# Kernel tuning notes

Hardware: AMD Instinct MI355X
Metric: run time of the kernel (lower is better)

## Reference

```python
import jax, jax.numpy as jnp
import numpy as np

NUM_HEADS = 12

def setup_inputs() -> dict:
    key = jax.random.key(0)
    k1, k2, k3 = jax.random.split(key, 3)
    B, N, C = 8, 1024, 768
    x = jax.random.normal(k1, (B, N, C), dtype=jnp.float32)
    w_qkv = jax.random.normal(k2, (C, 3 * C), dtype=jnp.float32) * (C ** -0.5)
    w_proj = jax.random.normal(k3, (C, C), dtype=jnp.float32) * (C ** -0.5)
    b_proj = jnp.zeros((C,), dtype=jnp.float32)
    return {"x": x, "w_qkv": w_qkv, "w_proj": w_proj, "b_proj": b_proj}

def reference(x, w_qkv, w_proj, b_proj):
    B, N, C = x.shape
    H = NUM_HEADS
    D = C // H  # head_dim
    qkv = jnp.einsum('bnc,ce->bne', x, w_qkv)  # [B,N,3C]
    qkv = qkv.reshape(B, N, 3, H, D).transpose(2, 0, 3, 1, 4)  # [3,B,H,N,D]
    q, k, v = qkv[0], qkv[1], qkv[2]
    scale = D ** -0.5
    att = jax.nn.softmax(jnp.einsum('bhnd,bhmd->bhnm', q, k) * scale, axis=-1)
    out = jnp.einsum('bhnm,bhmd->bhnd', att, v)  # [B,H,N,D]
    out = out.transpose(0, 2, 1, 3).reshape(B, N, C)
    return jnp.einsum('bnc,cd->bnd', out, w_proj) + b_proj
```

## Files before the change

kernel.cpp:

```cpp
#include <hip/hip_runtime.h>

constexpr int Bb = 8, Nn = 1024, Cc = 768, Hh = 12, Dd = 64;
constexpr int Mtot = Bb * Nn;
constexpr int QKVN = 3 * Cc;
constexpr int BH = Bb * Hh;

typedef __attribute__((ext_vector_type(8))) short short8b;
typedef __attribute__((ext_vector_type(4))) float f32x4;
typedef __attribute__((ext_vector_type(4))) unsigned short u16x4;

__device__ inline unsigned short bf16_hi(float f) {
  unsigned int u = __float_as_uint(f);
  unsigned int r = (u + 0x7FFFu + ((u >> 16) & 1u)) >> 16;
  return (unsigned short)r;
}
__device__ inline float bf16_to_f32(unsigned short h) {
  return __uint_as_float(((unsigned int)h) << 16);
}

__global__ __launch_bounds__(256)
void transpose_split(const float* __restrict__ in, unsigned short* __restrict__ Th,
                     unsigned short* __restrict__ Tl, int K, int N) {
  __shared__ float tile[32][33];
  const int tx = threadIdx.x & 31;
  const int ty = threadIdx.x >> 5;
  const int gk = blockIdx.y * 32;
  const int gn = blockIdx.x * 32;

  #pragma unroll
  for (int i = 0; i < 4; ++i) {
    int k = gk + ty + 8 * i;
    tile[ty + 8 * i][tx] = in[(size_t)k * N + gn + tx];
  }
  __syncthreads();
  #pragma unroll
  for (int i = 0; i < 4; ++i) {
    int n = gn + ty + 8 * i;
    float v = tile[tx][ty + 8 * i];
    unsigned short h = bf16_hi(v);
    float fl = v - bf16_to_f32(h);
    Th[(size_t)n * K + gk + tx] = h;
    Tl[(size_t)n * K + gk + tx] = bf16_hi(fl);
  }
}

template <int EPI>
__global__ __launch_bounds__(256)
void gemm_mfma(const float* __restrict__ A, const unsigned short* __restrict__ BTh,
               const unsigned short* __restrict__ BTl, const float* __restrict__ bias,
               float* __restrict__ Cout, int K, int Ncols) {
  constexpr int LDH = 40;
  __shared__ unsigned short Ah[128][LDH], Al[128][LDH];
  __shared__ unsigned short Bh[128][LDH], Bl[128][LDH];

  const int tid = threadIdx.x;
  const int lane = tid & 63;
  const int w = tid >> 6;
  const int wm = (w & 1) * 64, wn = (w >> 1) * 64;
  const int m0 = blockIdx.y * 128, n0 = blockIdx.x * 128;

  const int srow = tid >> 1;
  const int sko = (tid & 1) * 16;

  f32x4 acc[4][4];
  #pragma unroll
  for (int i = 0; i < 4; ++i)
    #pragma unroll
    for (int j = 0; j < 4; ++j) acc[i][j] = (f32x4)0.f;

  const int lr = lane & 15;
  const int lk = (lane >> 4) * 8;

  for (int k0 = 0; k0 < K; k0 += 32) {
    __syncthreads();
    {
      const float* ap = &A[(size_t)(m0 + srow) * K + k0 + sko];
      #pragma unroll
      for (int i = 0; i < 4; ++i) {
        float4 v = *(const float4*)&ap[4 * i];
        u16x4 h, l;
        float f[4] = {v.x, v.y, v.z, v.w};
        #pragma unroll
        for (int e = 0; e < 4; ++e) {
          unsigned short hh = bf16_hi(f[e]);
          h[e] = hh;
          l[e] = bf16_hi(f[e] - bf16_to_f32(hh));
        }
        *(u16x4*)&Ah[srow][sko + 4 * i] = h;
        *(u16x4*)&Al[srow][sko + 4 * i] = l;
      }
    }
    {
      const unsigned short* bhp = &BTh[(size_t)(n0 + srow) * K + k0 + sko];
      const unsigned short* blp = &BTl[(size_t)(n0 + srow) * K + k0 + sko];
      *(short8b*)&Bh[srow][sko]     = *(const short8b*)bhp;
      *(short8b*)&Bh[srow][sko + 8] = *(const short8b*)(bhp + 8);
      *(short8b*)&Bl[srow][sko]     = *(const short8b*)blp;
      *(short8b*)&Bl[srow][sko + 8] = *(const short8b*)(blp + 8);
    }
    __syncthreads();

    short8b ahf[4], alf[4], bhf[4], blf[4];
    #pragma unroll
    for (int mi = 0; mi < 4; ++mi) {
      ahf[mi] = *(const short8b*)&Ah[wm + mi * 16 + lr][lk];
      alf[mi] = *(const short8b*)&Al[wm + mi * 16 + lr][lk];
    }
    #pragma unroll
    for (int nj = 0; nj < 4; ++nj) {
      bhf[nj] = *(const short8b*)&Bh[wn + nj * 16 + lr][lk];
      blf[nj] = *(const short8b*)&Bl[wn + nj * 16 + lr][lk];
    }
    #pragma unroll
    for (int mi = 0; mi < 4; ++mi)
      #pragma unroll
      for (int nj = 0; nj < 4; ++nj) {
        acc[mi][nj] = __builtin_amdgcn_mfma_f32_16x16x32_bf16(
            ahf[mi], bhf[nj], acc[mi][nj], 0, 0, 0);
        acc[mi][nj] = __builtin_amdgcn_mfma_f32_16x16x32_bf16(
            ahf[mi], blf[nj], acc[mi][nj], 0, 0, 0);
        acc[mi][nj] = __builtin_amdgcn_mfma_f32_16x16x32_bf16(
            alf[mi], bhf[nj], acc[mi][nj], 0, 0, 0);
      }
  }

  #pragma unroll
  for (int mi = 0; mi < 4; ++mi) {
    #pragma unroll
    for (int nj = 0; nj < 4; ++nj) {
      #pragma unroll
      for (int r = 0; r < 4; ++r) {
        int m = m0 + wm + mi * 16 + (lane >> 4) * 4 + r;
        int n = n0 + wn + nj * 16 + lr;
        float v = acc[mi][nj][r];
        if (EPI == 0) {
          int t = n0 / Cc;
          int rem = n - t * Cc;
          int h = rem >> 6, d = rem & 63;
          int bI = m >> 10, nI = m & 1023;
          Cout[(((size_t)t * BH + bI * Hh + h) * Nn + nI) * Dd + d] = v;
        } else {
          Cout[(size_t)m * Cc + n] = v + bias[n];
        }
      }
    }
  }
}

__global__ __launch_bounds__(256)
void attn_mfma(const float* __restrict__ qkv_ws, float* __restrict__ aout) {
  constexpr int LDH2 = 72;
  __shared__ unsigned short Qh[64][LDH2], Ql[64][LDH2];
  __shared__ unsigned short Ksh[64][LDH2], Ksl[64][LDH2];
  __shared__ unsigned short Vth[64][LDH2], Vtl[64][LDH2];
  __shared__ unsigned short Ph[64][LDH2], Pl[64][LDH2];

  const int bid = blockIdx.x;
  const int bh = bid >> 4, qt = bid & 15;
  const int b = bh / Hh, h = bh % Hh;
  const int tid = threadIdx.x;
  const int lane = tid & 63;
  const int wv = tid >> 6;
  const int q0 = wv * 16;
  const int qp = lane & 15;
  const int g  = lane >> 4;

  const float* Qg = qkv_ws + ((size_t)bh * Nn + qt * 64) * Dd;
  const float* Kg = qkv_ws + ((size_t)(BH + bh) * Nn) * Dd;
  const float* Vg = qkv_ws + ((size_t)(2 * BH + bh) * Nn) * Dd;
  const float scale = 0.125f;

  #pragma unroll
  for (int s = 0; s < 4; ++s) {
    int f = s * 256 + tid;
    int row = f >> 4, c4 = (f & 15) * 4;
    float4 v = *(const float4*)&Qg[row * 64 + c4];
    float fv[4] = {v.x, v.y, v.z, v.w};
    u16x4 hh, ll;
    #pragma unroll
    for (int e = 0; e < 4; ++e) {
      unsigned short x = bf16_hi(fv[e]);
      hh[e] = x; ll[e] = bf16_hi(fv[e] - bf16_to_f32(x));
    }
    *(u16x4*)&Qh[row][c4] = hh;
    *(u16x4*)&Ql[row][c4] = ll;
  }
  __syncthreads();
  short8b qfh[2], qfl[2];
  #pragma unroll
  for (int ks = 0; ks < 2; ++ks) {
    qfh[ks] = *(const short8b*)&Qh[q0 + qp][ks * 32 + g * 8];
    qfl[ks] = *(const short8b*)&Ql[q0 + qp][ks * 32 + g * 8];
  }

  f32x4 acc_o[4];
  #pragma unroll
  for (int dt = 0; dt < 4; ++dt) acc_o[dt] = (f32x4)0.f;
  float mrun = -1e30f, lrun = 0.f;

  for (int kt = 0; kt < 16; ++kt) {
    __syncthreads();
    #pragma unroll
    for (int s = 0; s < 4; ++s) {
      int f = s * 256 + tid;
      int row = f >> 4, c4 = (f & 15) * 4;
      float4 v = *(const float4*)&Kg[(size_t)(kt * 64 + row) * 64 + c4];
      float fv[4] = {v.x, v.y, v.z, v.w};
      u16x4 hh, ll;
      #pragma unroll
      for (int e = 0; e < 4; ++e) {
        unsigned short x = bf16_hi(fv[e]);
        hh[e] = x; ll[e] = bf16_hi(fv[e] - bf16_to_f32(x));
      }
      *(u16x4*)&Ksh[row][c4] = hh;
      *(u16x4*)&Ksl[row][c4] = ll;
    }
    #pragma unroll
    for (int s = 0; s < 2; ++s) {
      int f = s * 256 + tid;
      int kv2 = (f >> 4) * 2, c4 = (f & 15) * 4;
      float4 v0 = *(const float4*)&Vg[(size_t)(kt * 64 + kv2) * 64 + c4];
      float4 v1 = *(const float4*)&Vg[(size_t)(kt * 64 + kv2 + 1) * 64 + c4];
      float a0[4] = {v0.x, v0.y, v0.z, v0.w};
      float a1[4] = {v1.x, v1.y, v1.z, v1.w};
      #pragma unroll
      for (int e = 0; e < 4; ++e) {
        unsigned short h0 = bf16_hi(a0[e]), h1 = bf16_hi(a1[e]);
        unsigned short l0 = bf16_hi(a0[e] - bf16_to_f32(h0));
        unsigned short l1 = bf16_hi(a1[e] - bf16_to_f32(h1));
        *(unsigned int*)&Vth[c4 + e][kv2] = (unsigned)h0 | ((unsigned)h1 << 16);
        *(unsigned int*)&Vtl[c4 + e][kv2] = (unsigned)l0 | ((unsigned)l1 << 16);
      }
    }
    __syncthreads();

    f32x4 sacc[4];
    #pragma unroll
    for (int kb = 0; kb < 4; ++kb) sacc[kb] = (f32x4)0.f;
    #pragma unroll
    for (int kb = 0; kb < 4; ++kb) {
      #pragma unroll
      for (int ks = 0; ks < 2; ++ks) {
        short8b kfh = *(const short8b*)&Ksh[kb * 16 + qp][ks * 32 + g * 8];
        short8b kfl = *(const short8b*)&Ksl[kb * 16 + qp][ks * 32 + g * 8];
        sacc[kb] = __builtin_amdgcn_mfma_f32_16x16x32_bf16(kfh, qfh[ks], sacc[kb], 0, 0, 0);
        sacc[kb] = __builtin_amdgcn_mfma_f32_16x16x32_bf16(kfh, qfl[ks], sacc[kb], 0, 0, 0);
        sacc[kb] = __builtin_amdgcn_mfma_f32_16x16x32_bf16(kfl, qfh[ks], sacc[kb], 0, 0, 0);
      }
    }

    float sv[16];
    #pragma unroll
    for (int kb = 0; kb < 4; ++kb)
      #pragma unroll
      for (int r = 0; r < 4; ++r) sv[kb * 4 + r] = sacc[kb][r] * scale;
    float tmax = sv[0];
    #pragma unroll
    for (int i = 1; i < 16; ++i) tmax = fmaxf(tmax, sv[i]);
    tmax = fmaxf(tmax, __shfl_xor(tmax, 16));
    tmax = fmaxf(tmax, __shfl_xor(tmax, 32));
    float mn = fmaxf(mrun, tmax);
    float corr = __expf(mrun - mn);
    float pv[16];
    float psum = 0.f;
    #pragma unroll
    for (int i = 0; i < 16; ++i) { pv[i] = __expf(sv[i] - mn); psum += pv[i]; }
    psum += __shfl_xor(psum, 16);
    psum += __shfl_xor(psum, 32);
    lrun = lrun * corr + psum;
    mrun = mn;
    #pragma unroll
    for (int r = 0; r < 4; ++r) {
      float cr = __shfl(corr, g * 4 + r);
      #pragma unroll
      for (int dt = 0; dt < 4; ++dt) acc_o[dt][r] *= cr;
    }

    #pragma unroll
    for (int kb = 0; kb < 4; ++kb) {
      unsigned short ph[4], plo[4];
      #pragma unroll
      for (int r = 0; r < 4; ++r) {
        ph[r] = bf16_hi(pv[kb * 4 + r]);
        plo[r] = bf16_hi(pv[kb * 4 + r] - bf16_to_f32(ph[r]));
      }
      int base = kb * 16 + g * 4;
      *(unsigned int*)&Ph[q0 + qp][base]     = (unsigned)ph[0] | ((unsigned)ph[1] << 16);
      *(unsigned int*)&Ph[q0 + qp][base + 2] = (unsigned)ph[2] | ((unsigned)ph[3] << 16);
      *(unsigned int*)&Pl[q0 + qp][base]     = (unsigned)plo[0] | ((unsigned)plo[1] << 16);
      *(unsigned int*)&Pl[q0 + qp][base + 2] = (unsigned)plo[2] | ((unsigned)plo[3] << 16);
    }
    __syncthreads();

    short8b pfh[2], pfl[2];
    #pragma unroll
    for (int ks = 0; ks < 2; ++ks) {
      pfh[ks] = *(const short8b*)&Ph[q0 + qp][ks * 32 + g * 8];
      pfl[ks] = *(const short8b*)&Pl[q0 + qp][ks * 32 + g * 8];
    }
    #pragma unroll
    for (int dt = 0; dt < 4; ++dt) {
      #pragma unroll
      for (int ks = 0; ks < 2; ++ks) {
        short8b vfh = *(const short8b*)&Vth[dt * 16 + qp][ks * 32 + g * 8];
        short8b vfl = *(const short8b*)&Vtl[dt * 16 + qp][ks * 32 + g * 8];
        acc_o[dt] = __builtin_amdgcn_mfma_f32_16x16x32_bf16(pfh[ks], vfh, acc_o[dt], 0, 0, 0);
        acc_o[dt] = __builtin_amdgcn_mfma_f32_16x16x32_bf16(pfh[ks], vfl, acc_o[dt], 0, 0, 0);
        acc_o[dt] = __builtin_amdgcn_mfma_f32_16x16x32_bf16(pfl[ks], vfh, acc_o[dt], 0, 0, 0);
      }
    }
  }

  float linv = 1.0f / lrun;
  #pragma unroll
  for (int r = 0; r < 4; ++r) {
    float lr = __shfl(linv, g * 4 + r);
    int q = qt * 64 + q0 + 4 * g + r;
    #pragma unroll
    for (int dt = 0; dt < 4; ++dt) {
      aout[((size_t)(b * Nn + q)) * Cc + h * 64 + dt * 16 + qp] = acc_o[dt][r] * lr;
    }
  }
}

extern "C" void kernel_launch(void* const* d_in, const int* in_sizes, int n_in,
                              void* d_out, int out_size, void* d_ws, size_t ws_size,
                              hipStream_t stream) {
  const float* x      = (const float*)d_in[0];
  const float* w_qkv  = (const float*)d_in[1];
  const float* w_proj = (const float*)d_in[2];
  const float* b_proj = (const float*)d_in[3];
  float* out = (float*)d_out;

  char* ws = (char*)d_ws;
  float* qkv_ws           = (float*)ws;
  unsigned short* wprojTh = (unsigned short*)ws;
  unsigned short* wprojTl = (unsigned short*)(ws + 1179648);
  unsigned short* wqkvTh  = (unsigned short*)(ws + 75497472);
  unsigned short* wqkvTl  = (unsigned short*)(ws + 79036416);
  float* aout             = (float*)(ws + 75497472);

  transpose_split<<<dim3(QKVN / 32, Cc / 32), 256, 0, stream>>>(w_qkv, wqkvTh, wqkvTl, Cc, QKVN);

  gemm_mfma<0><<<dim3(QKVN / 128, Mtot / 128), 256, 0, stream>>>(
      x, wqkvTh, wqkvTl, nullptr, qkv_ws, Cc, QKVN);

  attn_mfma<<<BH * (Nn / 64), 256, 0, stream>>>(qkv_ws, aout);

  transpose_split<<<dim3(Cc / 32, Cc / 32), 256, 0, stream>>>(w_proj, wprojTh, wprojTl, Cc, Cc);

  gemm_mfma<1><<<dim3(Cc / 128, Mtot / 128), 256, 0, stream>>>(
      aout, wprojTh, wprojTl, b_proj, out, Cc, Cc);
}
```

Measured before the change: 406.9 us.

## Emit pre-split bf16 hi/lo Q/K/V planes from QKV GEMM epilogue

The QKV GEMM epilogue now splits each fp32 result into bf16 high and low halves and writes six planes, with V stored already transposed. The attention kernel loads those planes directly: Q fragments come straight from global memory and K/V tiles are staged with vector copies, so the per-tile float-to-bf16 split and the V transpose are gone. The P buffer now reuses the K shared tile, behind an extra barrier, which cuts LDS use and may allow higher occupancy. In exchange the GEMM epilogue does more work, using scattered 2-byte stores for Q/K and 8-byte stores for V.

```diff
diff --git a/kernel.cpp b/kernel.cpp
--- a/kernel.cpp
+++ b/kernel.cpp
@@ -4,6 +4,7 @@
 constexpr int Mtot = Bb * Nn;
 constexpr int QKVN = 3 * Cc;
 constexpr int BH = Bb * Hh;
+constexpr size_t PLANE = (size_t)BH * Nn * Dd;
 
 typedef __attribute__((ext_vector_type(8))) short short8b;
 typedef __attribute__((ext_vector_type(4))) float f32x4;
@@ -48,7 +49,7 @@
 __global__ __launch_bounds__(256)
 void gemm_mfma(const float* __restrict__ A, const unsigned short* __restrict__ BTh,
                const unsigned short* __restrict__ BTl, const float* __restrict__ bias,
-               float* __restrict__ Cout, int K, int Ncols) {
+               float* __restrict__ Cout, unsigned short* __restrict__ planes, int K) {
   constexpr int LDH = 40;
   __shared__ unsigned short Ah[128][LDH], Al[128][LDH];
   __shared__ unsigned short Bh[128][LDH], Bl[128][LDH];
@@ -124,36 +125,73 @@
       }
   }
 
-  #pragma unroll
-  for (int mi = 0; mi < 4; ++mi) {
-    #pragma unroll
-    for (int nj = 0; nj < 4; ++nj) {
-      #pragma unroll
-      for (int r = 0; r < 4; ++r) {
-        int m = m0 + wm + mi * 16 + (lane >> 4) * 4 + r;
-        int n = n0 + wn + nj * 16 + lr;
-        float v = acc[mi][nj][r];
-        if (EPI == 0) {
-          int t = n0 / Cc;
-          int rem = n - t * Cc;
-          int h = rem >> 6, d = rem & 63;
-          int bI = m >> 10, nI = m & 1023;
-          Cout[(((size_t)t * BH + bI * Hh + h) * Nn + nI) * Dd + d] = v;
+  if (EPI == 0) {
+    const int t = n0 / Cc;
+    unsigned short* Hp = planes + (size_t)(2 * t) * PLANE;
+    unsigned short* Lp = planes + (size_t)(2 * t + 1) * PLANE;
+    #pragma unroll
+    for (int mi = 0; mi < 4; ++mi) {
+      const int mbase = m0 + wm + mi * 16 + (lane >> 4) * 4;
+      const int bI = mbase >> 10;
+      const int nI0 = mbase & 1023;
+      #pragma unroll
+      for (int nj = 0; nj < 4; ++nj) {
+        const int n = n0 + wn + nj * 16 + lr;
+        const int rem = n - t * Cc;
+        const int hh = rem >> 6, d = rem & 63;
+        const size_t bhI = (size_t)(bI * Hh + hh);
+        unsigned short vh4[4], vl4[4];
+        #pragma unroll
+        for (int r = 0; r < 4; ++r) {
+          float v = acc[mi][nj][r];
+          vh4[r] = bf16_hi(v);
+          vl4[r] = bf16_hi(v - bf16_to_f32(vh4[r]));
+        }
+        if (t < 2) {
+          #pragma unroll
+          for (int r = 0; r < 4; ++r) {
+            size_t idx = (bhI * Nn + nI0 + r) * Dd + d;
+            Hp[idx] = vh4[r];
+            Lp[idx] = vl4[r];
+          }
         } else {
-          Cout[(size_t)m * Cc + n] = v + bias[n];
+          u16x4 ph, pl;
+          #pragma unroll
+          for (int r = 0; r < 4; ++r) { ph[r] = vh4[r]; pl[r] = vl4[r]; }
+          size_t idx = (bhI * Dd + d) * Nn + nI0;
+          *(u16x4*)&Hp[idx] = ph;
+          *(u16x4*)&Lp[idx] = pl;
         }
       }
     }
+  } else {
+    #pragma unroll
+    for (int mi = 0; mi < 4; ++mi) {
+      #pragma unroll
+      for (int nj = 0; nj < 4; ++nj) {
+        #pragma unroll
+        for (int r = 0; r < 4; ++r) {
+          int m = m0 + wm + mi * 16 + (lane >> 4) * 4 + r;
+          int n = n0 + wn + nj * 16 + lr;
+          Cout[(size_t)m * Cc + n] = acc[mi][nj][r] + bias[n];
+        }
+      }
+    }
   }
 }
 
 __global__ __launch_bounds__(256)
-void attn_mfma(const float* __restrict__ qkv_ws, float* __restrict__ aout) {
+void attn_mfma(const unsigned short* __restrict__ planes, float* __restrict__ aout) {
   constexpr int LDH2 = 72;
-  __shared__ unsigned short Qh[64][LDH2], Ql[64][LDH2];
-  __shared__ unsigned short Ksh[64][LDH2], Ksl[64][LDH2];
+  __shared__ unsigned short KPh[64][LDH2], KPl[64][LDH2];
   __shared__ unsigned short Vth[64][LDH2], Vtl[64][LDH2];
-  __shared__ unsigned short Ph[64][LDH2], Pl[64][LDH2];
+
+  const unsigned short* Qh_p = planes;
+  const unsigned short* Ql_p = planes + PLANE;
+  const unsigned short* Kh_p = planes + 2 * PLANE;
+  const unsigned short* Kl_p = planes + 3 * PLANE;
+  const unsigned short* Vth_p = planes + 4 * PLANE;
+  const unsigned short* Vtl_p = planes + 5 * PLANE;
 
   const int bid = blockIdx.x;
   const int bh = bid >> 4, qt = bid & 15;
@@ -165,32 +203,17 @@
   const int qp = lane & 15;
   const int g  = lane >> 4;
 
-  const float* Qg = qkv_ws + ((size_t)bh * Nn + qt * 64) * Dd;
-  const float* Kg = qkv_ws + ((size_t)(BH + bh) * Nn) * Dd;
-  const float* Vg = qkv_ws + ((size_t)(2 * BH + bh) * Nn) * Dd;
+  const int srow = tid >> 2;
+  const int sc16 = (tid & 3) * 16;
+
   const float scale = 0.125f;
 
-  #pragma unroll
-  for (int s = 0; s < 4; ++s) {
-    int f = s * 256 + tid;
-    int row = f >> 4, c4 = (f & 15) * 4;
-    float4 v = *(const float4*)&Qg[row * 64 + c4];
-    float fv[4] = {v.x, v.y, v.z, v.w};
-    u16x4 hh, ll;
-    #pragma unroll
-    for (int e = 0; e < 4; ++e) {
-      unsigned short x = bf16_hi(fv[e]);
-      hh[e] = x; ll[e] = bf16_hi(fv[e] - bf16_to_f32(x));
-    }
-    *(u16x4*)&Qh[row][c4] = hh;
-    *(u16x4*)&Ql[row][c4] = ll;
-  }
-  __syncthreads();
+  const size_t qoff = ((size_t)bh * Nn + qt * 64 + q0 + qp) * Dd;
   short8b qfh[2], qfl[2];
   #pragma unroll
   for (int ks = 0; ks < 2; ++ks) {
-    qfh[ks] = *(const short8b*)&Qh[q0 + qp][ks * 32 + g * 8];
-    qfl[ks] = *(const short8b*)&Ql[q0 + qp][ks * 32 + g * 8];
+    qfh[ks] = *(const short8b*)&Qh_p[qoff + ks * 32 + g * 8];
+    qfl[ks] = *(const short8b*)&Ql_p[qoff + ks * 32 + g * 8];
   }
 
   f32x4 acc_o[4];
@@ -200,37 +223,21 @@
 
   for (int kt = 0; kt < 16; ++kt) {
     __syncthreads();
-    #pragma unroll
-    for (int s = 0; s < 4; ++s) {
-      int f = s * 256 + tid;
-      int row = f >> 4, c4 = (f & 15) * 4;
-      float4 v = *(const float4*)&Kg[(size_t)(kt * 64 + row) * 64 + c4];
-      float fv[4] = {v.x, v.y, v.z, v.w};
-      u16x4 hh, ll;
-      #pragma unroll
-      for (int e = 0; e < 4; ++e) {
-        unsigned short x = bf16_hi(fv[e]);
-        hh[e] = x; ll[e] = bf16_hi(fv[e] - bf16_to_f32(x));
-      }
-      *(u16x4*)&Ksh[row][c4] = hh;
-      *(u16x4*)&Ksl[row][c4] = ll;
-    }
-    #pragma unroll
-    for (int s = 0; s < 2; ++s) {
-      int f = s * 256 + tid;
-      int kv2 = (f >> 4) * 2, c4 = (f & 15) * 4;
-      float4 v0 = *(const float4*)&Vg[(size_t)(kt * 64 + kv2) * 64 + c4];
-      float4 v1 = *(const float4*)&Vg[(size_t)(kt * 64 + kv2 + 1) * 64 + c4];
-      float a0[4] = {v0.x, v0.y, v0.z, v0.w};
-      float a1[4] = {v1.x, v1.y, v1.z, v1.w};
-      #pragma unroll
-      for (int e = 0; e < 4; ++e) {
-        unsigned short h0 = bf16_hi(a0[e]), h1 = bf16_hi(a1[e]);
-        unsigned short l0 = bf16_hi(a0[e] - bf16_to_f32(h0));
-        unsigned short l1 = bf16_hi(a1[e] - bf16_to_f32(h1));
-        *(unsigned int*)&Vth[c4 + e][kv2] = (unsigned)h0 | ((unsigned)h1 << 16);
-        *(unsigned int*)&Vtl[c4 + e][kv2] = (unsigned)l0 | ((unsigned)l1 << 16);
-      }
+    {
+      const unsigned short* kh = &Kh_p[((size_t)bh * Nn + kt * 64 + srow) * Dd + sc16];
+      const unsigned short* kl = &Kl_p[((size_t)bh * Nn + kt * 64 + srow) * Dd + sc16];
+      *(short8b*)&KPh[srow][sc16]     = *(const short8b*)kh;
+      *(short8b*)&KPh[srow][sc16 + 8] = *(const short8b*)(kh + 8);
+      *(short8b*)&KPl[srow][sc16]     = *(const short8b*)kl;
+      *(short8b*)&KPl[srow][sc16 + 8] = *(const short8b*)(kl + 8);
+    }
+    {
+      const unsigned short* vh = &Vth_p[((size_t)bh * Dd + srow) * Nn + kt * 64 + sc16];
+      const unsigned short* vl = &Vtl_p[((size_t)bh * Dd + srow) * Nn + kt * 64 + sc16];
+      *(short8b*)&Vth[srow][sc16]     = *(const short8b*)vh;
+      *(short8b*)&Vth[srow][sc16 + 8] = *(const short8b*)(vh + 8);
+      *(short8b*)&Vtl[srow][sc16]     = *(const short8b*)vl;
+      *(short8b*)&Vtl[srow][sc16 + 8] = *(const short8b*)(vl + 8);
     }
     __syncthreads();
 
@@ -241,8 +248,8 @@
     for (int kb = 0; kb < 4; ++kb) {
       #pragma unroll
       for (int ks = 0; ks < 2; ++ks) {
-        short8b kfh = *(const short8b*)&Ksh[kb * 16 + qp][ks * 32 + g * 8];
-        short8b kfl = *(const short8b*)&Ksl[kb * 16 + qp][ks * 32 + g * 8];
+        short8b kfh = *(const short8b*)&KPh[kb * 16 + qp][ks * 32 + g * 8];
+        short8b kfl = *(const short8b*)&KPl[kb * 16 + qp][ks * 32 + g * 8];
         sacc[kb] = __builtin_amdgcn_mfma_f32_16x16x32_bf16(kfh, qfh[ks], sacc[kb], 0, 0, 0);
         sacc[kb] = __builtin_amdgcn_mfma_f32_16x16x32_bf16(kfh, qfl[ks], sacc[kb], 0, 0, 0);
         sacc[kb] = __builtin_amdgcn_mfma_f32_16x16x32_bf16(kfl, qfh[ks], sacc[kb], 0, 0, 0);
@@ -276,6 +283,7 @@
       for (int dt = 0; dt < 4; ++dt) acc_o[dt][r] *= cr;
     }
 
+    __syncthreads();
     #pragma unroll
     for (int kb = 0; kb < 4; ++kb) {
       unsigned short ph[4], plo[4];
@@ -285,18 +293,18 @@
         plo[r] = bf16_hi(pv[kb * 4 + r] - bf16_to_f32(ph[r]));
       }
       int base = kb * 16 + g * 4;
-      *(unsigned int*)&Ph[q0 + qp][base]     = (unsigned)ph[0] | ((unsigned)ph[1] << 16);
-      *(unsigned int*)&Ph[q0 + qp][base + 2] = (unsigned)ph[2] | ((unsigned)ph[3] << 16);
-      *(unsigned int*)&Pl[q0 + qp][base]     = (unsigned)plo[0] | ((unsigned)plo[1] << 16);
-      *(unsigned int*)&Pl[q0 + qp][base + 2] = (unsigned)plo[2] | ((unsigned)plo[3] << 16);
+      *(unsigned int*)&KPh[q0 + qp][base]     = (unsigned)ph[0] | ((unsigned)ph[1] << 16);
+      *(unsigned int*)&KPh[q0 + qp][base + 2] = (unsigned)ph[2] | ((unsigned)ph[3] << 16);
+      *(unsigned int*)&KPl[q0 + qp][base]     = (unsigned)plo[0] | ((unsigned)plo[1] << 16);
+      *(unsigned int*)&KPl[q0 + qp][base + 2] = (unsigned)plo[2] | ((unsigned)plo[3] << 16);
     }
     __syncthreads();
 
     short8b pfh[2], pfl[2];
     #pragma unroll
     for (int ks = 0; ks < 2; ++ks) {
-      pfh[ks] = *(const short8b*)&Ph[q0 + qp][ks * 32 + g * 8];
-      pfl[ks] = *(const short8b*)&Pl[q0 + qp][ks * 32 + g * 8];
+      pfh[ks] = *(const short8b*)&KPh[q0 + qp][ks * 32 + g * 8];
+      pfl[ks] = *(const short8b*)&KPl[q0 + qp][ks * 32 + g * 8];
     }
     #pragma unroll
     for (int dt = 0; dt < 4; ++dt) {
@@ -333,7 +341,7 @@
   float* out = (float*)d_out;
 
   char* ws = (char*)d_ws;
-  float* qkv_ws           = (float*)ws;
+  unsigned short* planes  = (unsigned short*)ws;
   unsigned short* wprojTh = (unsigned short*)ws;
   unsigned short* wprojTl = (unsigned short*)(ws + 1179648);
   unsigned short* wqkvTh  = (unsigned short*)(ws + 75497472);
@@ -343,12 +351,12 @@
   transpose_split<<<dim3(QKVN / 32, Cc / 32), 256, 0, stream>>>(w_qkv, wqkvTh, wqkvTl, Cc, QKVN);
 
   gemm_mfma<0><<<dim3(QKVN / 128, Mtot / 128), 256, 0, stream>>>(
-      x, wqkvTh, wqkvTl, nullptr, qkv_ws, Cc, QKVN);
-
-  attn_mfma<<<BH * (Nn / 64), 256, 0, stream>>>(qkv_ws, aout);
+      x, wqkvTh, wqkvTl, nullptr, nullptr, planes, Cc);
+
+  attn_mfma<<<BH * (Nn / 64), 256, 0, stream>>>(planes, aout);
 
   transpose_split<<<dim3(Cc / 32, Cc / 32), 256, 0, stream>>>(w_proj, wprojTh, wprojTl, Cc, Cc);
 
   gemm_mfma<1><<<dim3(Cc / 128, Mtot / 128), 256, 0, stream>>>(
-      aout, wprojTh, wprojTl, b_proj, out, Cc, Cc);
-}
+      aout, wprojTh, wprojTl, b_proj, out, nullptr, Cc);
+}
```

Result: faster. 362.4 us (-10.9%).
